# Kernel optimization log

Measured on AMD Instinct MI355X. Metric: run time of the kernel, lower is better.

## Reference

```python
import jax, jax.numpy as jnp
import numpy as np

N_EMBD = 768
HEAD_SIZE = 64
B, T = 32, 1024


def setup_inputs() -> dict:
    key = jax.random.key(0)
    k1, k2, k3, k4 = jax.random.split(key, 4)
    x = jax.random.normal(k1, (B, T, N_EMBD), dtype=jnp.float32)
    Wq = jax.random.normal(k2, (N_EMBD, HEAD_SIZE), dtype=jnp.float32) * 0.02
    Wk = jax.random.normal(k3, (N_EMBD, HEAD_SIZE), dtype=jnp.float32) * 0.02
    Wv = jax.random.normal(k4, (N_EMBD, HEAD_SIZE), dtype=jnp.float32) * 0.02
    return {"x": x, "Wq": Wq, "Wk": Wk, "Wv": Wv}


def _apply_rope(q, k):
    # q, k: [B, T, D]; interleaved (even/odd) RoPE exactly as the torch source
    seq_len, dim = q.shape[-2], q.shape[-1]
    pos = jnp.arange(seq_len, dtype=jnp.float32)[:, None]                      # [T, 1]
    div_term = jnp.exp(jnp.arange(0, dim, 2, dtype=jnp.float32) * (-jnp.log(10000.0) / dim))  # [D/2]
    sin_emb = jnp.sin(pos * div_term)                                          # [T, D/2]
    cos_emb = jnp.cos(pos * div_term)                                          # [T, D/2]

    def rot(t):
        te, to = t[..., ::2], t[..., 1::2]
        re = te * cos_emb - to * sin_emb
        ro = te * sin_emb + to * cos_emb
        # interleave back: [..., T, D/2, 2] -> [..., T, D]
        return jnp.stack([re, ro], axis=-1).reshape(t.shape)

    return rot(q), rot(k)


def reference(x, Wq, Wk, Wv):
    Bx, Tx, C = x.shape  # C == n_embd
    q = x @ Wq  # [B, T, D]
    k = x @ Wk
    v = x @ Wv
    q, k = _apply_rope(q, k)
    # NOTE: source scales by C**-0.5 where C = n_embd, not head_size
    wei = jnp.einsum('btd,bsd->bts', q, k) * (C ** -0.5)  # [B, T, T]
    causal = jnp.tril(jnp.ones((Tx, Tx), dtype=bool))
    wei = jnp.where(causal, wei, -jnp.inf)
    wei = jax.nn.softmax(wei, axis=-1)
    # dropout is identity in eval mode
    out = jnp.einsum('bts,bsd->btd', wei, v)  # [B, T, D]
    return out
```

## Files before the change

kernel.cpp:

```cpp
#include <hip/hip_runtime.h>
#include <cmath>

#define B 32
#define T 1024
#define CDIM 768
#define D 64
#define SCALE 0.03608439182435161f
#define XSTR 72

typedef short bf16x8 __attribute__((ext_vector_type(8)));
typedef float f32x4 __attribute__((ext_vector_type(4)));
typedef unsigned short u16x8 __attribute__((ext_vector_type(8)));

__device__ inline ushort f2bf(float f) {
  union { float f; unsigned u; } v{f};
  unsigned r = (v.u + 0x7FFFu + ((v.u >> 16) & 1u)) >> 16;
  return (ushort)r;
}

__global__ __launch_bounds__(256) void wt_prep(
    const float* __restrict__ Wq, const float* __restrict__ Wk,
    const float* __restrict__ Wv, ushort* __restrict__ Wt)
{
  const int n   = blockIdx.x;
  const int sel = n >> 6, col = n & 63;
  const float* W = (sel == 0) ? Wq : (sel == 1) ? Wk : Wv;
  const float sc = (sel == 0) ? SCALE : 1.f;
  for (int k = threadIdx.x; k < CDIM; k += 256)
    Wt[(size_t)n * CDIM + k] = f2bf(W[(size_t)k * D + col] * sc);
}

__global__ __launch_bounds__(512, 4) void proj_mfma(
    const float* __restrict__ x,
    const ushort* __restrict__ Wt,
    ushort* __restrict__ qkv)
{
  const int t    = threadIdx.x;
  const int lane = t & 63;
  const int wid  = t >> 6;
  const int ln16 = lane & 15;
  const int quad = lane >> 4;
  const int mt   = wid & 3;
  const int nh   = wid >> 2;
  const int row0 = blockIdx.x * 64;

  __shared__ ushort Xs[2][64 * XSTR];
  __shared__ ushort Ws[2][192 * XSTR];

  f32x4 acc[6];
  #pragma unroll
  for (int nt = 0; nt < 6; ++nt) acc[nt] = (f32x4){0.f, 0.f, 0.f, 0.f};

  float4 xp[2][2];
  u16x8  wp[2][3];

  auto load_stage = [&](int s, int set) {
    const int k0 = s * 64;
    #pragma unroll
    for (int it = 0; it < 2; ++it) {
      int slot = it * 512 + t, row = slot >> 4, kq = slot & 15;
      xp[set][it] = *(const float4*)(x + (size_t)(row0 + row) * CDIM + k0 + kq * 4);
    }
    #pragma unroll
    for (int it = 0; it < 3; ++it) {
      int slot = it * 512 + t, n = slot >> 3, kb = slot & 7;
      wp[set][it] = *(const u16x8*)(Wt + (size_t)n * CDIM + k0 + kb * 8);
    }
  };

  load_stage(0, 0);
  load_stage(1, 1);
  int buf = 0;
  for (int s = 0; s < CDIM / 64; ++s) {
    const int set = s & 1;
    #pragma unroll
    for (int it = 0; it < 2; ++it) {
      int slot = it * 512 + t, row = slot >> 4, kq = slot & 15;
      ushort4 bv;
      bv.x = f2bf(xp[set][it].x); bv.y = f2bf(xp[set][it].y);
      bv.z = f2bf(xp[set][it].z); bv.w = f2bf(xp[set][it].w);
      *(ushort4*)&Xs[buf][row * XSTR + kq * 4] = bv;
    }
    #pragma unroll
    for (int it = 0; it < 3; ++it) {
      int slot = it * 512 + t, n = slot >> 3, kb = slot & 7;
      *(u16x8*)&Ws[buf][n * XSTR + kb * 8] = wp[set][it];
    }
    __syncthreads();
    if (s + 2 < CDIM / 64) load_stage(s + 2, set);

    #pragma unroll
    for (int ks = 0; ks < 2; ++ks) {
      bf16x8 a = *(const bf16x8*)&Xs[buf][(mt * 16 + ln16) * XSTR + ks * 32 + quad * 8];
      #pragma unroll
      for (int nt = 0; nt < 6; ++nt) {
        const int ntg = nh * 6 + nt;
        bf16x8 bb = *(const bf16x8*)&Ws[buf][(ntg * 16 + ln16) * XSTR + ks * 32 + quad * 8];
        acc[nt] = __builtin_amdgcn_mfma_f32_16x16x32_bf16(a, bb, acc[nt], 0, 0, 0);
      }
    }
    buf ^= 1;
  }

  #pragma unroll
  for (int nt = 0; nt < 6; ++nt) {
    const int ntg = nh * 6 + nt;
    const int sel = ntg >> 2;
    const int d   = (ntg & 3) * 16 + ln16;
    ushort* outb = qkv + (size_t)sel * (B * T * D);
    if (sel < 2) {
      const float freq = __expf((float)(d & 62) * (-0.14391156855801f));
      const float sgn  = (d & 1) ? 1.f : -1.f;
      #pragma unroll
      for (int reg = 0; reg < 4; ++reg) {
        int rowg = row0 + mt * 16 + quad * 4 + reg;
        float s, c;
        __sincosf((float)(rowg & (T - 1)) * freq, &s, &c);
        float val = acc[nt][reg];
        float partner = __shfl_xor(val, 1, 64);
        outb[(size_t)rowg * D + d] = f2bf(fmaf(sgn * partner, s, val * c));
      }
    } else {
      #pragma unroll
      for (int reg = 0; reg < 4; ++reg) {
        int rowg = row0 + mt * 16 + quad * 4 + reg;
        outb[(size_t)rowg * D + d] = f2bf(acc[nt][reg]);
      }
    }
  }
}

__global__ __launch_bounds__(256) void attn_mfma(
    const ushort* __restrict__ qg,
    const ushort* __restrict__ kg,
    const ushort* __restrict__ vg,
    float* __restrict__ out)
{
  const int t    = threadIdx.x;
  const int lane = t & 63;
  const int wid  = t >> 6;
  const int ln16 = lane & 15;
  const int quad = lane >> 4;
  const int l    = (int)blockIdx.x;
  const int b    = l & 31;
  const int r    = l >> 5;
  const int qt   = (r < 8) ? r : 23 - r;

  __shared__ ushort Ks[2][64 * XSTR];
  __shared__ ushort Vt[2][64 * XSTR];
  __shared__ ushort Pl[64 * XSTR];

  bf16x8 qf[2];
  {
    const ushort* qrow = qg + (size_t)(b * T + qt * 64 + wid * 16 + ln16) * D;
    qf[0] = *(const bf16x8*)(qrow + quad * 8);
    qf[1] = *(const bf16x8*)(qrow + quad * 8 + 32);
  }

  f32x4 O[4];
  #pragma unroll
  for (int nt = 0; nt < 4; ++nt) O[nt] = (f32x4){0.f, 0.f, 0.f, 0.f};
  float l_sum = 0.f;

  const int kb = t & 15, db = t >> 4;
  const int d0 = db * 4, kk0 = kb * 4;

  u16x8  kp[2];
  ushort4 vp[4];
  auto load_kv = [&](int kt) {
    #pragma unroll
    for (int i = 0; i < 2; ++i) {
      int slot = i * 256 + t, row = slot >> 3, dblk = slot & 7;
      kp[i] = *(const u16x8*)(kg + (size_t)(b * T + kt * 64 + row) * D + dblk * 8);
    }
    #pragma unroll
    for (int i = 0; i < 4; ++i)
      vp[i] = *(const ushort4*)(vg + (size_t)(b * T + kt * 64 + kk0 + i) * D + d0);
  };

  load_kv(0);
  int buf = 0;
  for (int kt = 0; kt <= qt; ++kt) {
    #pragma unroll
    for (int i = 0; i < 2; ++i) {
      int slot = i * 256 + t, row = slot >> 3, dblk = slot & 7;
      *(u16x8*)&Ks[buf][row * XSTR + dblk * 8] = kp[i];
    }
    const ushort* vpe = (const ushort*)vp;
    #pragma unroll
    for (int j = 0; j < 4; ++j) {
      ushort4 c;
      c.x = vpe[0 * 4 + j]; c.y = vpe[1 * 4 + j];
      c.z = vpe[2 * 4 + j]; c.w = vpe[3 * 4 + j];
      *(ushort4*)&Vt[buf][(d0 + j) * XSTR + kk0] = c;
    }
    __syncthreads();
    if (kt < qt) load_kv(kt + 1);

    f32x4 s[4];
    #pragma unroll
    for (int mt = 0; mt < 4; ++mt) s[mt] = (f32x4){0.f, 0.f, 0.f, 0.f};
    #pragma unroll
    for (int ks = 0; ks < 2; ++ks)
      #pragma unroll
      for (int mt = 0; mt < 4; ++mt) {
        bf16x8 kf = *(const bf16x8*)&Ks[buf][(mt * 16 + ln16) * XSTR + quad * 8 + ks * 32];
        s[mt] = __builtin_amdgcn_mfma_f32_16x16x32_bf16(kf, qf[ks], s[mt], 0, 0, 0);
      }

    if (kt == qt) {
      const int ql = wid * 16 + ln16;
      #pragma unroll
      for (int mt = 0; mt < 4; ++mt)
        #pragma unroll
        for (int reg = 0; reg < 4; ++reg)
          if (mt * 16 + quad * 4 + reg > ql) s[mt][reg] = -1e30f;
    }

    float psum = 0.f;
    #pragma unroll
    for (int mt = 0; mt < 4; ++mt) {
      float p0 = __expf(s[mt][0]), p1 = __expf(s[mt][1]);
      float p2 = __expf(s[mt][2]), p3 = __expf(s[mt][3]);
      psum += (p0 + p1) + (p2 + p3);
      ushort4 pk;
      pk.x = f2bf(p0); pk.y = f2bf(p1); pk.z = f2bf(p2); pk.w = f2bf(p3);
      *(ushort4*)&Pl[(wid * 16 + ln16) * XSTR + mt * 16 + quad * 4] = pk;
    }
    psum += __shfl_xor(psum, 16, 64);
    psum += __shfl_xor(psum, 32, 64);
    l_sum += psum;

    bf16x8 pa[2];
    pa[0] = *(const bf16x8*)&Pl[(wid * 16 + ln16) * XSTR + quad * 8];
    pa[1] = *(const bf16x8*)&Pl[(wid * 16 + ln16) * XSTR + quad * 8 + 32];
    #pragma unroll
    for (int ks = 0; ks < 2; ++ks)
      #pragma unroll
      for (int nt = 0; nt < 4; ++nt) {
        bf16x8 vf = *(const bf16x8*)&Vt[buf][(nt * 16 + ln16) * XSTR + quad * 8 + ks * 32];
        O[nt] = __builtin_amdgcn_mfma_f32_16x16x32_bf16(pa[ks], vf, O[nt], 0, 0, 0);
      }
    buf ^= 1;
  }

  float inv = 1.f / l_sum;
  #pragma unroll
  for (int reg = 0; reg < 4; ++reg) {
    float iv = __shfl(inv, quad * 4 + reg, 64);
    size_t row = (size_t)(b * T + qt * 64 + wid * 16 + quad * 4 + reg) * D;
    #pragma unroll
    for (int nt = 0; nt < 4; ++nt)
      out[row + nt * 16 + ln16] = O[nt][reg] * iv;
  }
}

extern "C" void kernel_launch(void* const* d_in, const int* in_sizes, int n_in,
                              void* d_out, int out_size, void* d_ws, size_t ws_size,
                              hipStream_t stream) {
  const float* x  = (const float*)d_in[0];
  const float* Wq = (const float*)d_in[1];
  const float* Wk = (const float*)d_in[2];
  const float* Wv = (const float*)d_in[3];
  float* outp = (float*)d_out;

  ushort* qkv = (ushort*)d_ws;
  ushort* Wt  = qkv + (size_t)3 * B * T * D;

  wt_prep<<<dim3(192), dim3(256), 0, stream>>>(Wq, Wk, Wv, Wt);
  proj_mfma<<<dim3((B * T) / 64), dim3(512), 0, stream>>>(x, Wt, qkv);
  attn_mfma<<<dim3(T / 64 * B), dim3(256), 0, stream>>>(
      qkv, qkv + (size_t)B * T * D, qkv + 2 * (size_t)B * T * D, outp);
}
```

Baseline: 180.1 us.

## Fuse weight prep, projection and attention into one cooperative kernel with grid syncs

Merges the three kernels into a single cooperative launch of 512 blocks of 512 threads, separated by grid-wide syncs, to remove the launch gaps between them. The attention phase runs on only half of each block's threads (the other 256 idle), and s_setprio is added around the MFMA sections. The three-kernel path remains as a fallback if the cooperative launch fails. Grid syncs add cost, and idling half the threads during attention may lower throughput in that phase.

```diff
diff --git a/kernel.cpp b/kernel.cpp
--- a/kernel.cpp
+++ b/kernel.cpp
@@ -1,5 +1,8 @@
 #include <hip/hip_runtime.h>
+#include <hip/hip_cooperative_groups.h>
 #include <cmath>
+
+namespace cg = cooperative_groups;
 
 #define B 32
 #define T 1024
@@ -16,6 +19,264 @@
   union { float f; unsigned u; } v{f};
   unsigned r = (v.u + 0x7FFFu + ((v.u >> 16) & 1u)) >> 16;
   return (ushort)r;
+}
+
+__global__ __launch_bounds__(512, 4) void fused(
+    const float* __restrict__ x,
+    const float* __restrict__ Wq, const float* __restrict__ Wk,
+    const float* __restrict__ Wv,
+    float* __restrict__ out,
+    ushort* __restrict__ qkv,
+    ushort* __restrict__ Wt)
+{
+  __shared__ ushort SMEM[36864];
+  const int t = threadIdx.x;
+
+  if (blockIdx.x < 192) {
+    const int n = blockIdx.x, sel = n >> 6, col = n & 63;
+    const float* W = (sel == 0) ? Wq : (sel == 1) ? Wk : Wv;
+    const float sc = (sel == 0) ? SCALE : 1.f;
+    for (int k = t; k < CDIM; k += 512)
+      Wt[(size_t)n * CDIM + k] = f2bf(W[(size_t)k * D + col] * sc);
+  }
+  __threadfence();
+  cg::this_grid().sync();
+
+  {
+    const int lane = t & 63;
+    const int wid  = t >> 6;
+    const int ln16 = lane & 15;
+    const int quad = lane >> 4;
+    const int mt   = wid & 3;
+    const int nh   = wid >> 2;
+    const int row0 = blockIdx.x * 64;
+
+    ushort* Xs0 = SMEM;
+    ushort* Ws0 = SMEM + 2 * 64 * XSTR;
+
+    f32x4 acc[6];
+    #pragma unroll
+    for (int nt = 0; nt < 6; ++nt) acc[nt] = (f32x4){0.f, 0.f, 0.f, 0.f};
+
+    float4 xp[2][2];
+    u16x8  wp[2][3];
+
+    auto load_stage = [&](int s, int set) {
+      const int k0 = s * 64;
+      #pragma unroll
+      for (int it = 0; it < 2; ++it) {
+        int slot = it * 512 + t, row = slot >> 4, kq = slot & 15;
+        xp[set][it] = *(const float4*)(x + (size_t)(row0 + row) * CDIM + k0 + kq * 4);
+      }
+      #pragma unroll
+      for (int it = 0; it < 3; ++it) {
+        int slot = it * 512 + t, n = slot >> 3, kb = slot & 7;
+        wp[set][it] = *(const u16x8*)(Wt + (size_t)n * CDIM + k0 + kb * 8);
+      }
+    };
+
+    load_stage(0, 0);
+    load_stage(1, 1);
+    int buf = 0;
+    for (int s = 0; s < CDIM / 64; ++s) {
+      const int set = s & 1;
+      ushort* Xs = Xs0 + buf * 64 * XSTR;
+      ushort* Ws = Ws0 + buf * 192 * XSTR;
+      #pragma unroll
+      for (int it = 0; it < 2; ++it) {
+        int slot = it * 512 + t, row = slot >> 4, kq = slot & 15;
+        ushort4 bv;
+        bv.x = f2bf(xp[set][it].x); bv.y = f2bf(xp[set][it].y);
+        bv.z = f2bf(xp[set][it].z); bv.w = f2bf(xp[set][it].w);
+        *(ushort4*)&Xs[row * XSTR + kq * 4] = bv;
+      }
+      #pragma unroll
+      for (int it = 0; it < 3; ++it) {
+        int slot = it * 512 + t, n = slot >> 3, kb = slot & 7;
+        *(u16x8*)&Ws[n * XSTR + kb * 8] = wp[set][it];
+      }
+      __syncthreads();
+      if (s + 2 < CDIM / 64) load_stage(s + 2, set);
+
+      #pragma unroll
+      for (int ks = 0; ks < 2; ++ks) {
+        bf16x8 a = *(const bf16x8*)&Xs[(mt * 16 + ln16) * XSTR + ks * 32 + quad * 8];
+        #pragma unroll
+        for (int nt = 0; nt < 6; ++nt) {
+          const int ntg = nh * 6 + nt;
+          bf16x8 bb = *(const bf16x8*)&Ws[(ntg * 16 + ln16) * XSTR + ks * 32 + quad * 8];
+          acc[nt] = __builtin_amdgcn_mfma_f32_16x16x32_bf16(a, bb, acc[nt], 0, 0, 0);
+        }
+      }
+      __syncthreads();
+      buf ^= 1;
+    }
+
+    #pragma unroll
+    for (int nt = 0; nt < 6; ++nt) {
+      const int ntg = nh * 6 + nt;
+      const int sel = ntg >> 2;
+      const int d   = (ntg & 3) * 16 + ln16;
+      ushort* outb = qkv + (size_t)sel * (B * T * D);
+      if (sel < 2) {
+        const float freq = __expf((float)(d & 62) * (-0.14391156855801f));
+        const float sgn  = (d & 1) ? 1.f : -1.f;
+        #pragma unroll
+        for (int reg = 0; reg < 4; ++reg) {
+          int rowg = row0 + mt * 16 + quad * 4 + reg;
+          float s, c;
+          __sincosf((float)(rowg & (T - 1)) * freq, &s, &c);
+          float val = acc[nt][reg];
+          float partner = __shfl_xor(val, 1, 64);
+          outb[(size_t)rowg * D + d] = f2bf(fmaf(sgn * partner, s, val * c));
+        }
+      } else {
+        #pragma unroll
+        for (int reg = 0; reg < 4; ++reg) {
+          int rowg = row0 + mt * 16 + quad * 4 + reg;
+          outb[(size_t)rowg * D + d] = f2bf(acc[nt][reg]);
+        }
+      }
+    }
+  }
+  __threadfence();
+  cg::this_grid().sync();
+
+  {
+    const bool act = t < 256;
+    const int lane = t & 63;
+    const int wid  = t >> 6;
+    const int ln16 = lane & 15;
+    const int quad = lane >> 4;
+    const int l    = (int)blockIdx.x;
+    const int b    = l & 31;
+    const int r    = l >> 5;
+    const int qt   = (r < 8) ? r : 23 - r;
+
+    ushort* Ks0 = SMEM;
+    ushort* Vt0 = SMEM + 2 * 64 * XSTR;
+    ushort* Pl  = SMEM + 4 * 64 * XSTR;
+
+    const ushort* qg = qkv;
+    const ushort* kg = qkv + (size_t)B * T * D;
+    const ushort* vg = qkv + 2 * (size_t)B * T * D;
+
+    bf16x8 qf[2];
+    if (act) {
+      const ushort* qrow = qg + (size_t)(b * T + qt * 64 + wid * 16 + ln16) * D;
+      qf[0] = *(const bf16x8*)(qrow + quad * 8);
+      qf[1] = *(const bf16x8*)(qrow + quad * 8 + 32);
+    }
+
+    f32x4 O[4];
+    #pragma unroll
+    for (int nt = 0; nt < 4; ++nt) O[nt] = (f32x4){0.f, 0.f, 0.f, 0.f};
+    float l_sum = 0.f;
+
+    const int kb = t & 15, db = t >> 4;
+    const int d0 = (db & 15) * 4, kk0 = kb * 4;
+
+    u16x8  kp[2];
+    ushort4 vp[4];
+    auto load_kv = [&](int kt) {
+      #pragma unroll
+      for (int i = 0; i < 2; ++i) {
+        int slot = i * 256 + t, row = slot >> 3, dblk = slot & 7;
+        kp[i] = *(const u16x8*)(kg + (size_t)(b * T + kt * 64 + row) * D + dblk * 8);
+      }
+      #pragma unroll
+      for (int i = 0; i < 4; ++i)
+        vp[i] = *(const ushort4*)(vg + (size_t)(b * T + kt * 64 + kk0 + i) * D + d0);
+    };
+
+    if (act) load_kv(0);
+    int buf = 0;
+    for (int kt = 0; kt <= qt; ++kt) {
+      ushort* Ks = Ks0 + buf * 64 * XSTR;
+      ushort* Vt = Vt0 + buf * 64 * XSTR;
+      if (act) {
+        #pragma unroll
+        for (int i = 0; i < 2; ++i) {
+          int slot = i * 256 + t, row = slot >> 3, dblk = slot & 7;
+          *(u16x8*)&Ks[row * XSTR + dblk * 8] = kp[i];
+        }
+        const ushort* vpe = (const ushort*)vp;
+        #pragma unroll
+        for (int j = 0; j < 4; ++j) {
+          ushort4 c;
+          c.x = vpe[0 * 4 + j]; c.y = vpe[1 * 4 + j];
+          c.z = vpe[2 * 4 + j]; c.w = vpe[3 * 4 + j];
+          *(ushort4*)&Vt[(d0 + j) * XSTR + kk0] = c;
+        }
+      }
+      __syncthreads();
+      if (act) {
+        if (kt < qt) load_kv(kt + 1);
+
+        f32x4 s[4];
+        #pragma unroll
+        for (int mt = 0; mt < 4; ++mt) s[mt] = (f32x4){0.f, 0.f, 0.f, 0.f};
+        __builtin_amdgcn_s_setprio(1);
+        #pragma unroll
+        for (int ks = 0; ks < 2; ++ks)
+          #pragma unroll
+          for (int mt = 0; mt < 4; ++mt) {
+            bf16x8 kf = *(const bf16x8*)&Ks[(mt * 16 + ln16) * XSTR + quad * 8 + ks * 32];
+            s[mt] = __builtin_amdgcn_mfma_f32_16x16x32_bf16(kf, qf[ks], s[mt], 0, 0, 0);
+          }
+        __builtin_amdgcn_s_setprio(0);
+
+        if (kt == qt) {
+          const int ql = wid * 16 + ln16;
+          #pragma unroll
+          for (int mt = 0; mt < 4; ++mt)
+            #pragma unroll
+            for (int reg = 0; reg < 4; ++reg)
+              if (mt * 16 + quad * 4 + reg > ql) s[mt][reg] = -1e30f;
+        }
+
+        float psum = 0.f;
+        #pragma unroll
+        for (int mt = 0; mt < 4; ++mt) {
+          float p0 = __expf(s[mt][0]), p1 = __expf(s[mt][1]);
+          float p2 = __expf(s[mt][2]), p3 = __expf(s[mt][3]);
+          psum += (p0 + p1) + (p2 + p3);
+          ushort4 pk;
+          pk.x = f2bf(p0); pk.y = f2bf(p1); pk.z = f2bf(p2); pk.w = f2bf(p3);
+          *(ushort4*)&Pl[(wid * 16 + ln16) * XSTR + mt * 16 + quad * 4] = pk;
+        }
+        psum += __shfl_xor(psum, 16, 64);
+        psum += __shfl_xor(psum, 32, 64);
+        l_sum += psum;
+
+        bf16x8 pa[2];
+        pa[0] = *(const bf16x8*)&Pl[(wid * 16 + ln16) * XSTR + quad * 8];
+        pa[1] = *(const bf16x8*)&Pl[(wid * 16 + ln16) * XSTR + quad * 8 + 32];
+        __builtin_amdgcn_s_setprio(1);
+        #pragma unroll
+        for (int ks = 0; ks < 2; ++ks)
+          #pragma unroll
+          for (int nt = 0; nt < 4; ++nt) {
+            bf16x8 vf = *(const bf16x8*)&Vt[(nt * 16 + ln16) * XSTR + quad * 8 + ks * 32];
+            O[nt] = __builtin_amdgcn_mfma_f32_16x16x32_bf16(pa[ks], vf, O[nt], 0, 0, 0);
+          }
+        __builtin_amdgcn_s_setprio(0);
+      }
+      buf ^= 1;
+    }
+
+    if (act) {
+      float inv = 1.f / l_sum;
+      #pragma unroll
+      for (int reg = 0; reg < 4; ++reg) {
+        float iv = __shfl(inv, quad * 4 + reg, 64);
+        size_t row = (size_t)(b * T + qt * 64 + wid * 16 + quad * 4 + reg) * D;
+        #pragma unroll
+        for (int nt = 0; nt < 4; ++nt)
+          out[row + nt * 16 + ln16] = O[nt][reg] * iv;
+      }
+    }
+  }
 }
 
 __global__ __launch_bounds__(256) void wt_prep(
@@ -267,8 +528,15 @@
   ushort* qkv = (ushort*)d_ws;
   ushort* Wt  = qkv + (size_t)3 * B * T * D;
 
-  wt_prep<<<dim3(192), dim3(256), 0, stream>>>(Wq, Wk, Wv, Wt);
-  proj_mfma<<<dim3((B * T) / 64), dim3(512), 0, stream>>>(x, Wt, qkv);
-  attn_mfma<<<dim3(T / 64 * B), dim3(256), 0, stream>>>(
-      qkv, qkv + (size_t)B * T * D, qkv + 2 * (size_t)B * T * D, outp);
+  void* args[] = {(void*)&x, (void*)&Wq, (void*)&Wk, (void*)&Wv,
+                  (void*)&outp, (void*)&qkv, (void*)&Wt};
+  hipError_t err = hipLaunchCooperativeKernel(
+      (void*)fused, dim3(512), dim3(512), args, 0, stream);
+
+  if (err != hipSuccess) {
+    wt_prep<<<dim3(192), dim3(256), 0, stream>>>(Wq, Wk, Wv, Wt);
+    proj_mfma<<<dim3((B * T) / 64), dim3(512), 0, stream>>>(x, Wt, qkv);
+    attn_mfma<<<dim3(T / 64 * B), dim3(256), 0, stream>>>(
+        qkv, qkv + (size_t)B * T * D, qkv + 2 * (size_t)B * T * D, outp);
+  }
 }
```

Result: slower. 497.2 us (+176.1%).
